# Kernel tuning notes

Measured on AMD Instinct MI355X. Metric: run time of the kernel, lower is better.

## Reference

```python
import jax, jax.numpy as jnp
import numpy as np

B, N, D = 2, 4096, 1152   # batch, tokens, txt_dim == pix_dim (num_heads = 1)
RMS_EPS = 1e-8


def setup_inputs() -> dict:
    key = jax.random.key(0)
    ks = jax.random.split(key, 8)
    w = lambda k, shape: jax.random.normal(k, shape, dtype=jnp.float32) * 0.02
    return {
        "x": jax.random.normal(ks[0], (B, N, D), dtype=jnp.float32),
        "c": jax.random.normal(ks[1], (B, N, D), dtype=jnp.float32),
        "Wqkv_pix": w(ks[2], (3 * D, D)),      # nn.Linear(pix_dim, 3*pix_dim), no bias
        "Wqkv_text": w(ks[3], (3 * D, D)),     # nn.Linear(txt_dim, 3*txt_dim), no bias
        "sq_text": jnp.ones((D,), jnp.float32),
        "sk_text": jnp.ones((D,), jnp.float32),
        "sq_pix": jnp.ones((D,), jnp.float32),
        "sk_pix": jnp.ones((D,), jnp.float32),
        "Wproj_pix": w(ks[4], (D, 2 * D)),     # nn.Linear(dim, txt_dim)
        "bproj_pix": jnp.zeros((D,), jnp.float32),
        "Wproj_text": w(ks[5], (D, 2 * D)),    # nn.Linear(dim, pix_dim)
        "bproj_text": jnp.zeros((D,), jnp.float32),
    }


def _rms_norm(t, scale):
    # RMSNorm with p<0 path: L2 norm over last dim, rms = ||x|| * d^-0.5
    d = t.shape[-1]
    rms = jnp.linalg.norm(t, axis=-1, keepdims=True) * (d ** -0.5)
    return scale * (t / (rms + RMS_EPS))


def reference(x, c, Wqkv_pix, Wqkv_text, sq_text, sk_text, sq_pix, sk_pix,
              Wproj_pix, bproj_pix, Wproj_text, bproj_text):
    Bx, Nx, D1 = x.shape  # num_heads == 1, so (B, 1, N, d) == (B, N, d)
    # pix stream QKV (from x)
    qkv_pix = (x @ Wqkv_pix.T).reshape(Bx, Nx, 3, D1)
    q_pix, k_pix, v_pix = qkv_pix[:, :, 0], qkv_pix[:, :, 1], qkv_pix[:, :, 2]
    q_pix = _rms_norm(q_pix, sq_pix)
    k_pix = _rms_norm(k_pix, sk_pix)
    # text stream QKV: NOTE the original code applies qkv_text to x, not c
    qkv_text = (x @ Wqkv_text.T).reshape(Bx, Nx, 3, D1)
    q_text, k_text, v_text = qkv_text[:, :, 0], qkv_text[:, :, 1], qkv_text[:, :, 2]
    q_text = _rms_norm(q_text, sq_text)
    k_text = _rms_norm(k_text, sk_text)
    # concat text/pix along feature dim -> (B, N, 2D)
    q = jnp.concatenate([q_text, q_pix], axis=-1)
    k = jnp.concatenate([k_text, k_pix], axis=-1)
    v = jnp.concatenate([v_text, v_pix], axis=-1)
    scale = (2 * D1) ** -0.5  # head_dim = (txt_dim + pix_dim) / num_heads
    attn = jax.nn.softmax(jnp.einsum("bnd,bmd->bnm", q, k) * scale, axis=-1)
    z = jnp.einsum("bnm,bmd->bnd", attn, v)  # (B, N, 2D)
    x_out = z @ Wproj_pix.T + bproj_pix
    c_out = z @ Wproj_text.T + bproj_text
    return (x_out, c_out)
```

## Files before the change

### kernel.cpp

```cpp
#include <hip/hip_runtime.h>
#include <hip/hip_bf16.h>
#include <stdint.h>

using short8 = __attribute__((ext_vector_type(8))) short;
using f32x4  = __attribute__((ext_vector_type(4))) float;

#define DD 1152
#define ROW 6912

static __device__ __forceinline__ float bf2f(uint32_t h){
  union { uint32_t u; float f; } v; v.u = (h & 0xffffu) << 16; return v.f;
}
static __device__ __forceinline__ ushort f2bf(float f){
  union { float f; uint32_t u; } v; v.f = f;
  uint32_t r = (v.u + 0x7fffu + ((v.u >> 16) & 1u)) >> 16;
  return (ushort)r;
}
static __device__ __forceinline__ uint32_t pack2(float a, float b){
  return (uint32_t)f2bf(a) | ((uint32_t)f2bf(b) << 16);
}

static __device__ __forceinline__ void gload16(const void* g, void* l){
  __builtin_amdgcn_global_load_lds(
      (const __attribute__((address_space(1))) void*)g,
      (__attribute__((address_space(3))) void*)l, 16, 0, 0);
}

template<int EPI>
__global__ __launch_bounds__(512, 2)
void gemm256(const ushort* __restrict__ A, int lda,
             const ushort* __restrict__ Bm, int ldb,
             void* __restrict__ Cout, int ldc,
             int K, float alpha, int ntx, int row0,
             float* __restrict__ out0, float* __restrict__ out1,
             const float* __restrict__ bias0, const float* __restrict__ bias1)
{
  __shared__ __align__(16) ushort lds[65536];
  const int tid  = threadIdx.x;
  const int w    = tid >> 6, lane = tid & 63;
  const int wr   = w >> 2, wc = w & 3;

  const int nwg = gridDim.x;
  const int wg  = blockIdx.x;
  const int swz = (wg & 7) * (nwg >> 3) + (wg >> 3);
  const int tx = swz % ntx, ty = swz / ntx;
  const int m0 = ty * 256, n0 = tx * 256;

  const int srow = lane >> 2;
  const int scol = 8 * ((lane & 3) ^ ((lane >> 3) & 3));
  const int sgA  = w * 2;
  const ushort* gA0 = A  + (size_t)(m0 + sgA * 16 + srow) * lda + scol;
  const ushort* gA1 = gA0 + (size_t)16 * lda;
  const ushort* gB0 = Bm + (size_t)(n0 + sgA * 16 + srow) * ldb + scol;
  const ushort* gB1 = gB0 + (size_t)16 * ldb;

  auto stageAll = [&](int t, int bf) {
    ushort* Lb = lds + bf * 16384;
    gload16(gA0 + t * 32, Lb + sgA * 512);
    gload16(gA1 + t * 32, Lb + sgA * 512 + 512);
    gload16(gB0 + t * 32, Lb + 8192 + sgA * 512);
    gload16(gB1 + t * 32, Lb + 8192 + sgA * 512 + 512);
  };

  const int kq    = lane >> 4;
  const int rowA0 = wr * 128 + (lane & 15);
  const int adA   = rowA0 * 32 + 8 * (kq ^ ((rowA0 >> 1) & 3));
  const int rowB0 = wc * 64 + (lane & 15);
  const int adB   = rowB0 * 32 + 8 * (kq ^ ((rowB0 >> 1) & 3));

  f32x4 acc[8][4];
#pragma unroll
  for (int m = 0; m < 8; m++)
#pragma unroll
    for (int n = 0; n < 4; n++) acc[m][n] = f32x4{0.f, 0.f, 0.f, 0.f};

  const int nt = K >> 5;

  stageAll(0, 0); stageAll(1, 1); stageAll(2, 2);
  asm volatile("s_waitcnt vmcnt(8)" ::: "memory");
  __builtin_amdgcn_s_barrier();

  for (int t = 0; t < nt; ++t) {
    const ushort* Lb = lds + (t & 3) * 16384;
    short8 a0[4], b[4];
#pragma unroll
    for (int m = 0; m < 4; m++) a0[m] = *(const short8*)(Lb + adA + m * 512);
#pragma unroll
    for (int n = 0; n < 4; n++) b[n] = *(const short8*)(Lb + 8192 + adB + n * 512);
    if (t + 3 < nt) {
      ushort* Ld = lds + ((t + 3) & 3) * 16384;
      gload16(gA0 + (t + 3) * 32, Ld + sgA * 512);
      gload16(gA1 + (t + 3) * 32, Ld + sgA * 512 + 512);
    }
    __builtin_amdgcn_s_barrier();
    __builtin_amdgcn_s_setprio(1);
#pragma unroll
    for (int m = 0; m < 4; m++)
#pragma unroll
      for (int n = 0; n < 4; n++)
        acc[m][n] = __builtin_amdgcn_mfma_f32_16x16x32_bf16(a0[m], b[n], acc[m][n], 0, 0, 0);
    __builtin_amdgcn_s_setprio(0);

    short8 a1[4];
#pragma unroll
    for (int m = 0; m < 4; m++) a1[m] = *(const short8*)(Lb + adA + (m + 4) * 512);
    if (t + 3 < nt) {
      ushort* Ld = lds + ((t + 3) & 3) * 16384;
      gload16(gB0 + (t + 3) * 32, Ld + 8192 + sgA * 512);
      gload16(gB1 + (t + 3) * 32, Ld + 8192 + sgA * 512 + 512);
    }
    if      (t + 3 < nt) asm volatile("s_waitcnt vmcnt(8)" ::: "memory");
    else if (t + 2 < nt) asm volatile("s_waitcnt vmcnt(4)" ::: "memory");
    else                 asm volatile("s_waitcnt vmcnt(0)" ::: "memory");
    __builtin_amdgcn_s_barrier();
    __builtin_amdgcn_s_setprio(1);
#pragma unroll
    for (int m = 0; m < 4; m++)
#pragma unroll
      for (int n = 0; n < 4; n++)
        acc[m + 4][n] = __builtin_amdgcn_mfma_f32_16x16x32_bf16(a1[m], b[n], acc[m + 4][n], 0, 0, 0);
    __builtin_amdgcn_s_setprio(0);
  }

#pragma unroll
  for (int m = 0; m < 8; m++) {
#pragma unroll
    for (int v = 0; v < 4; v++) {
      const int row = m0 + wr * 128 + m * 16 + (lane >> 4) * 4 + v;
#pragma unroll
      for (int n = 0; n < 4; n++) {
        const int col = n0 + wc * 64 + n * 16 + (lane & 15);
        float val = acc[m][n][v] * alpha;
        if (EPI == 0) {
          ((ushort*)Cout)[(size_t)row * ldc + col] = f2bf(val);
        } else {
          const int orow = row0 + row;
          if (col < DD) out0[(size_t)orow * DD + col] = val + bias0[col];
          else          out1[(size_t)orow * DD + (col - DD)] = val + bias1[col - DD];
        }
      }
    }
  }
}

__global__ __launch_bounds__(256)
void cvt_f32_bf16(const float* __restrict__ src, ushort* __restrict__ dst, int n4)
{
  int stride = gridDim.x * blockDim.x;
  for (int i = blockIdx.x * blockDim.x + threadIdx.x; i < n4; i += stride) {
    float4 v = ((const float4*)src)[i];
    uint2 o;
    o.x = pack2(v.x, v.y);
    o.y = pack2(v.z, v.w);
    ((uint2*)dst)[i] = o;
  }
}

__global__ __launch_bounds__(256)
void rms_inplace(ushort* __restrict__ qkv,
                 const float* __restrict__ sq_text, const float* __restrict__ sq_pix,
                 const float* __restrict__ sk_text, const float* __restrict__ sk_pix)
{
  const int row = blockIdx.x;
  const int tid = threadIdx.x, wave = tid >> 6, lane = tid & 63;
  ushort* seg = qkv + (size_t)row * ROW + wave * 1152;
  const float* scale = (wave == 0) ? sq_text : (wave == 1) ? sq_pix
                     : (wave == 2) ? sk_text : sk_pix;
  float ss = 0.f;
  for (int g = lane; g < 144; g += 64) {
    uint4 p = *(const uint4*)(seg + g * 8);
    float f0 = bf2f(p.x), f1 = bf2f(p.x >> 16), f2 = bf2f(p.y), f3 = bf2f(p.y >> 16);
    float f4 = bf2f(p.z), f5 = bf2f(p.z >> 16), f6 = bf2f(p.w), f7 = bf2f(p.w >> 16);
    ss += f0*f0 + f1*f1 + f2*f2 + f3*f3 + f4*f4 + f5*f5 + f6*f6 + f7*f7;
  }
#pragma unroll
  for (int off = 32; off; off >>= 1) ss += __shfl_xor(ss, off);
  float rms = sqrtf(ss) * 0.0294627825f;
  float inv = 1.0f / (rms + 1e-8f);
  for (int g = lane; g < 144; g += 64) {
    int d0 = g * 8;
    uint4 p = *(const uint4*)(seg + d0);
    float f[8];
    f[0]=bf2f(p.x); f[1]=bf2f(p.x>>16); f[2]=bf2f(p.y); f[3]=bf2f(p.y>>16);
    f[4]=bf2f(p.z); f[5]=bf2f(p.z>>16); f[6]=bf2f(p.w); f[7]=bf2f(p.w>>16);
    uint4 o;
    o.x = pack2(f[0]*scale[d0+0]*inv, f[1]*scale[d0+1]*inv);
    o.y = pack2(f[2]*scale[d0+2]*inv, f[3]*scale[d0+3]*inv);
    o.z = pack2(f[4]*scale[d0+4]*inv, f[5]*scale[d0+5]*inv);
    o.w = pack2(f[6]*scale[d0+6]*inv, f[7]*scale[d0+7]*inv);
    *(uint4*)(seg + d0) = o;
  }
}

__global__ __launch_bounds__(256)
void transpose_v(const ushort* __restrict__ qkv, ushort* __restrict__ Vt)
{
  __shared__ ushort t[64][72];
  const int nb = blockIdx.x, db = blockIdx.y, b = blockIdx.z;
  const int tid = threadIdx.x;
  const int d0 = db * 64;
  const int srccol = 4608 + d0;
  const int rr = tid >> 3, cc = (tid & 7) * 8;
#pragma unroll
  for (int it = 0; it < 2; it++) {
    int r = rr + it * 32;
    uint4 p = *(const uint4*)(qkv + (size_t)(b * 4096 + nb * 64 + r) * ROW + srccol + cc);
    *(uint4*)&t[r][cc] = p;
  }
  __syncthreads();
#pragma unroll
  for (int it = 0; it < 2; it++) {
    int d = rr + it * 32;
    uint4 o;
    o.x = (uint32_t)t[cc+0][d] | ((uint32_t)t[cc+1][d] << 16);
    o.y = (uint32_t)t[cc+2][d] | ((uint32_t)t[cc+3][d] << 16);
    o.z = (uint32_t)t[cc+4][d] | ((uint32_t)t[cc+5][d] << 16);
    o.w = (uint32_t)t[cc+6][d] | ((uint32_t)t[cc+7][d] << 16);
    *(uint4*)(Vt + ((size_t)b * 2304 + d0 + d) * 4096 + nb * 64 + cc) = o;
  }
}

__global__ __launch_bounds__(256)
void softmax_bf16(ushort* __restrict__ S)
{
  const int row = blockIdx.x;
  ushort* sr = S + (size_t)row * 4096;
  const int tid = threadIdx.x, wave = tid >> 6, lane = tid & 63;
  __shared__ float red[8];
  uint4 p0 = ((const uint4*)sr)[tid * 2];
  uint4 p1 = ((const uint4*)sr)[tid * 2 + 1];
  float f[16];
  f[0]=bf2f(p0.x); f[1]=bf2f(p0.x>>16); f[2]=bf2f(p0.y); f[3]=bf2f(p0.y>>16);
  f[4]=bf2f(p0.z); f[5]=bf2f(p0.z>>16); f[6]=bf2f(p0.w); f[7]=bf2f(p0.w>>16);
  f[8]=bf2f(p1.x); f[9]=bf2f(p1.x>>16); f[10]=bf2f(p1.y); f[11]=bf2f(p1.y>>16);
  f[12]=bf2f(p1.z); f[13]=bf2f(p1.z>>16); f[14]=bf2f(p1.w); f[15]=bf2f(p1.w>>16);
  float mx = f[0];
#pragma unroll
  for (int j = 1; j < 16; j++) mx = fmaxf(mx, f[j]);
#pragma unroll
  for (int off = 32; off; off >>= 1) mx = fmaxf(mx, __shfl_xor(mx, off));
  if (lane == 0) red[wave] = mx;
  __syncthreads();
  mx = fmaxf(fmaxf(red[0], red[1]), fmaxf(red[2], red[3]));
  float s = 0.f;
#pragma unroll
  for (int j = 0; j < 16; j++) { f[j] = expf(f[j] - mx); s += f[j]; }
#pragma unroll
  for (int off = 32; off; off >>= 1) s += __shfl_xor(s, off);
  if (lane == 0) red[4 + wave] = s;
  __syncthreads();
  s = red[4] + red[5] + red[6] + red[7];
  float inv = 1.0f / s;
  uint4 o0, o1;
  o0.x = pack2(f[0]*inv, f[1]*inv);  o0.y = pack2(f[2]*inv, f[3]*inv);
  o0.z = pack2(f[4]*inv, f[5]*inv);  o0.w = pack2(f[6]*inv, f[7]*inv);
  o1.x = pack2(f[8]*inv, f[9]*inv);  o1.y = pack2(f[10]*inv, f[11]*inv);
  o1.z = pack2(f[12]*inv, f[13]*inv); o1.w = pack2(f[14]*inv, f[15]*inv);
  ((uint4*)sr)[tid * 2]     = o0;
  ((uint4*)sr)[tid * 2 + 1] = o1;
}

extern "C" void kernel_launch(void* const* d_in, const int* in_sizes, int n_in,
                              void* d_out, int out_size, void* d_ws, size_t ws_size,
                              hipStream_t stream)
{
  const float* x          = (const float*)d_in[0];
  const float* Wqkv_pix   = (const float*)d_in[2];
  const float* Wqkv_text  = (const float*)d_in[3];
  const float* sq_text    = (const float*)d_in[4];
  const float* sk_text    = (const float*)d_in[5];
  const float* sq_pix     = (const float*)d_in[6];
  const float* sk_pix     = (const float*)d_in[7];
  const float* Wproj_pix  = (const float*)d_in[8];
  const float* bproj_pix  = (const float*)d_in[9];
  const float* Wproj_text = (const float*)d_in[10];
  const float* bproj_text = (const float*)d_in[11];

  if (ws_size < 195166208ULL) return;
  char* ws = (char*)d_ws;
  ushort* QKV = (ushort*)(ws);
  ushort* Z   = (ushort*)(ws);
  ushort* Vt  = (ushort*)(ws + 113246208);
  ushort* S   = (ushort*)(ws + 150994944);
  ushort* Wpb = (ushort*)(ws + 184549376);
  ushort* xb  = (ushort*)(ws + 113246208);
  ushort* Wb  = (ushort*)(ws + 150994944);

  cvt_f32_bf16<<<2048, 256, 0, stream>>>(x, xb, 9437184 / 4);
  for (int t = 0; t < 3; t++) {
    cvt_f32_bf16<<<512, 256, 0, stream>>>(Wqkv_text + (size_t)t * 1327104,
                                          Wb + (size_t)(2 * t) * 1327104, 1327104 / 4);
    cvt_f32_bf16<<<512, 256, 0, stream>>>(Wqkv_pix + (size_t)t * 1327104,
                                          Wb + (size_t)(2 * t + 1) * 1327104, 1327104 / 4);
  }
  cvt_f32_bf16<<<512, 256, 0, stream>>>(Wproj_pix, Wpb, 2654208 / 4);
  cvt_f32_bf16<<<512, 256, 0, stream>>>(Wproj_text, Wpb + 2654208, 2654208 / 4);

  gemm256<0><<<dim3(864), 512, 0, stream>>>(xb, 1152, Wb, 1152, QKV, ROW,
                                            1152, 1.0f, 27, 0,
                                            nullptr, nullptr, nullptr, nullptr);
  rms_inplace<<<8192, 256, 0, stream>>>(QKV, sq_text, sq_pix, sk_text, sk_pix);
  {
    dim3 g(64, 36, 2);
    transpose_v<<<g, 256, 0, stream>>>(QKV, Vt);
  }

  const float scale = 1.0f / 48.0f;
  const size_t slab = (size_t)4096 * ROW;
  for (int b = 0; b < 2; b++) {
    const ushort* Qb = QKV + b * slab;
    const ushort* Kb = QKV + b * slab + 2304;
    const ushort* Vb = Vt + (size_t)b * 2304 * 4096;
    ushort* Zb = Z + (size_t)b * 4096 * 2304;
    gemm256<0><<<dim3(256), 512, 0, stream>>>(Qb, ROW, Kb, ROW, S, 4096,
                                              2304, scale, 16, 0,
                                              nullptr, nullptr, nullptr, nullptr);
    softmax_bf16<<<4096, 256, 0, stream>>>(S);
    gemm256<0><<<dim3(144), 512, 0, stream>>>(S, 4096, Vb, 4096, Zb, 2304,
                                              4096, 1.0f, 9, 0,
                                              nullptr, nullptr, nullptr, nullptr);
  }

  {
    float* out0 = (float*)d_out;
    float* out1 = out0 + 9437184;
    gemm256<2><<<dim3(288), 512, 0, stream>>>(Z, 2304, Wpb, 2304, nullptr, 0,
                                              2304, 1.0f, 9, 0,
                                              out0, out1, bproj_pix, bproj_text);
  }
}
```

Baseline: 755.3 us.

## Restructure GEMM main loop into four-quadrant schedule with K=64 tiles

Rewrites the 256x256 GEMM inner loop to use K-steps of 64 with the tile split into four 128x128 quadrants. Each quadrant is computed by all waves in turn while the next half-tiles stream into double-buffered LDS with a new XOR swizzle. This interleaves global loads with MFMA phases more finely and halves the number of loop iterations. It adds more barriers per iteration and changes the wave-to-output mapping, which could hurt if synchronisation dominates.

```diff
diff --git a/kernel.cpp b/kernel.cpp
--- a/kernel.cpp
+++ b/kernel.cpp
@@ -46,97 +46,151 @@
   const int tx = swz % ntx, ty = swz / ntx;
   const int m0 = ty * 256, n0 = tx * 256;
 
-  const int srow = lane >> 2;
-  const int scol = 8 * ((lane & 3) ^ ((lane >> 3) & 3));
-  const int sgA  = w * 2;
-  const ushort* gA0 = A  + (size_t)(m0 + sgA * 16 + srow) * lda + scol;
-  const ushort* gA1 = gA0 + (size_t)16 * lda;
-  const ushort* gB0 = Bm + (size_t)(n0 + sgA * 16 + srow) * ldb + scol;
-  const ushort* gB1 = gB0 + (size_t)16 * ldb;
-
-  auto stageAll = [&](int t, int bf) {
-    ushort* Lb = lds + bf * 16384;
-    gload16(gA0 + t * 32, Lb + sgA * 512);
-    gload16(gA1 + t * 32, Lb + sgA * 512 + 512);
-    gload16(gB0 + t * 32, Lb + 8192 + sgA * 512);
-    gload16(gB1 + t * 32, Lb + 8192 + sgA * 512 + 512);
+  const int sr = lane >> 3;
+  const int cc = 8 * ((lane & 7) ^ sr);
+  auto stageA = [&](int h, int tt) {
+    ushort* Ld = lds + ((tt & 1) * 2 + h) * 8192 + w * 1024;
+    const ushort* g = A + (size_t)(m0 + h * 128 + w * 16 + sr) * lda + tt * 64 + cc;
+    gload16(g, Ld);
+    gload16(g + (size_t)8 * lda, Ld + 512);
   };
-
-  const int kq    = lane >> 4;
-  const int rowA0 = wr * 128 + (lane & 15);
-  const int adA   = rowA0 * 32 + 8 * (kq ^ ((rowA0 >> 1) & 3));
-  const int rowB0 = wc * 64 + (lane & 15);
-  const int adB   = rowB0 * 32 + 8 * (kq ^ ((rowB0 >> 1) & 3));
-
-  f32x4 acc[8][4];
-#pragma unroll
-  for (int m = 0; m < 8; m++)
-#pragma unroll
-    for (int n = 0; n < 4; n++) acc[m][n] = f32x4{0.f, 0.f, 0.f, 0.f};
-
-  const int nt = K >> 5;
-
-  stageAll(0, 0); stageAll(1, 1); stageAll(2, 2);
-  asm volatile("s_waitcnt vmcnt(8)" ::: "memory");
+  auto stageB = [&](int h, int tt) {
+    ushort* Ld = lds + 32768 + ((tt & 1) * 2 + h) * 8192 + w * 1024;
+    const ushort* g = Bm + (size_t)(n0 + h * 128 + w * 16 + sr) * ldb + tt * 64 + cc;
+    gload16(g, Ld);
+    gload16(g + (size_t)8 * ldb, Ld + 512);
+  };
+
+  const int rowA = (wr * 64 + (lane & 15)) * 64;
+  const int rowB = (wc * 32 + (lane & 15)) * 64;
+  const int ck0  = 8 * (((lane >> 4) + 0) ^ (lane & 7));
+  const int ck1  = 8 * (((lane >> 4) + 4) ^ (lane & 7));
+
+  f32x4 acc0[4][2], acc1[4][2], acc2[4][2], acc3[4][2];
+#pragma unroll
+  for (int m = 0; m < 4; m++)
+#pragma unroll
+    for (int n = 0; n < 2; n++) {
+      acc0[m][n] = f32x4{0.f,0.f,0.f,0.f}; acc1[m][n] = f32x4{0.f,0.f,0.f,0.f};
+      acc2[m][n] = f32x4{0.f,0.f,0.f,0.f}; acc3[m][n] = f32x4{0.f,0.f,0.f,0.f};
+    }
+
+  const int nt = K >> 6;
+
+  stageA(0, 0); stageB(0, 0); stageA(1, 0); stageB(1, 0);
+  stageA(0, 1); stageB(0, 1);
+  asm volatile("s_waitcnt vmcnt(4)" ::: "memory");
   __builtin_amdgcn_s_barrier();
 
   for (int t = 0; t < nt; ++t) {
-    const ushort* Lb = lds + (t & 3) * 16384;
-    short8 a0[4], b[4];
-#pragma unroll
-    for (int m = 0; m < 4; m++) a0[m] = *(const short8*)(Lb + adA + m * 512);
-#pragma unroll
-    for (int n = 0; n < 4; n++) b[n] = *(const short8*)(Lb + 8192 + adB + n * 512);
-    if (t + 3 < nt) {
-      ushort* Ld = lds + ((t + 3) & 3) * 16384;
-      gload16(gA0 + (t + 3) * 32, Ld + sgA * 512);
-      gload16(gA1 + (t + 3) * 32, Ld + sgA * 512 + 512);
-    }
+    const ushort* LA = lds + (t & 1) * 16384;
+    const ushort* LB = LA + 32768;
+    short8 a[4][2], b[2][2];
+
+#pragma unroll
+    for (int m = 0; m < 4; m++) {
+      a[m][0] = *(const short8*)(LA + rowA + m * 1024 + ck0);
+      a[m][1] = *(const short8*)(LA + rowA + m * 1024 + ck1);
+    }
+#pragma unroll
+    for (int n = 0; n < 2; n++) {
+      b[n][0] = *(const short8*)(LB + rowB + n * 1024 + ck0);
+      b[n][1] = *(const short8*)(LB + rowB + n * 1024 + ck1);
+    }
+    if (t + 1 < nt) stageA(1, t + 1);
     __builtin_amdgcn_s_barrier();
     __builtin_amdgcn_s_setprio(1);
 #pragma unroll
     for (int m = 0; m < 4; m++)
 #pragma unroll
-      for (int n = 0; n < 4; n++)
-        acc[m][n] = __builtin_amdgcn_mfma_f32_16x16x32_bf16(a0[m], b[n], acc[m][n], 0, 0, 0);
+      for (int n = 0; n < 2; n++) {
+        acc0[m][n] = __builtin_amdgcn_mfma_f32_16x16x32_bf16(a[m][0], b[n][0], acc0[m][n], 0, 0, 0);
+        acc0[m][n] = __builtin_amdgcn_mfma_f32_16x16x32_bf16(a[m][1], b[n][1], acc0[m][n], 0, 0, 0);
+      }
     __builtin_amdgcn_s_setprio(0);
-
-    short8 a1[4];
-#pragma unroll
-    for (int m = 0; m < 4; m++) a1[m] = *(const short8*)(Lb + adA + (m + 4) * 512);
-    if (t + 3 < nt) {
-      ushort* Ld = lds + ((t + 3) & 3) * 16384;
-      gload16(gB0 + (t + 3) * 32, Ld + 8192 + sgA * 512);
-      gload16(gB1 + (t + 3) * 32, Ld + 8192 + sgA * 512 + 512);
-    }
-    if      (t + 3 < nt) asm volatile("s_waitcnt vmcnt(8)" ::: "memory");
-    else if (t + 2 < nt) asm volatile("s_waitcnt vmcnt(4)" ::: "memory");
-    else                 asm volatile("s_waitcnt vmcnt(0)" ::: "memory");
+    __builtin_amdgcn_s_barrier();
+
+#pragma unroll
+    for (int m = 0; m < 4; m++) {
+      a[m][0] = *(const short8*)(LA + 8192 + rowA + m * 1024 + ck0);
+      a[m][1] = *(const short8*)(LA + 8192 + rowA + m * 1024 + ck1);
+    }
+    if (t + 1 < nt) stageB(1, t + 1);
     __builtin_amdgcn_s_barrier();
     __builtin_amdgcn_s_setprio(1);
 #pragma unroll
     for (int m = 0; m < 4; m++)
 #pragma unroll
-      for (int n = 0; n < 4; n++)
-        acc[m + 4][n] = __builtin_amdgcn_mfma_f32_16x16x32_bf16(a1[m], b[n], acc[m + 4][n], 0, 0, 0);
+      for (int n = 0; n < 2; n++) {
+        acc1[m][n] = __builtin_amdgcn_mfma_f32_16x16x32_bf16(a[m][0], b[n][0], acc1[m][n], 0, 0, 0);
+        acc1[m][n] = __builtin_amdgcn_mfma_f32_16x16x32_bf16(a[m][1], b[n][1], acc1[m][n], 0, 0, 0);
+      }
     __builtin_amdgcn_s_setprio(0);
-  }
-
-#pragma unroll
-  for (int m = 0; m < 8; m++) {
-#pragma unroll
-    for (int v = 0; v < 4; v++) {
-      const int row = m0 + wr * 128 + m * 16 + (lane >> 4) * 4 + v;
-#pragma unroll
-      for (int n = 0; n < 4; n++) {
-        const int col = n0 + wc * 64 + n * 16 + (lane & 15);
-        float val = acc[m][n][v] * alpha;
-        if (EPI == 0) {
-          ((ushort*)Cout)[(size_t)row * ldc + col] = f2bf(val);
-        } else {
-          const int orow = row0 + row;
-          if (col < DD) out0[(size_t)orow * DD + col] = val + bias0[col];
-          else          out1[(size_t)orow * DD + (col - DD)] = val + bias1[col - DD];
+    __builtin_amdgcn_s_barrier();
+
+#pragma unroll
+    for (int m = 0; m < 4; m++) {
+      a[m][0] = *(const short8*)(LA + rowA + m * 1024 + ck0);
+      a[m][1] = *(const short8*)(LA + rowA + m * 1024 + ck1);
+    }
+#pragma unroll
+    for (int n = 0; n < 2; n++) {
+      b[n][0] = *(const short8*)(LB + 8192 + rowB + n * 1024 + ck0);
+      b[n][1] = *(const short8*)(LB + 8192 + rowB + n * 1024 + ck1);
+    }
+    if (t + 2 < nt) stageB(0, t + 2);
+    __builtin_amdgcn_s_barrier();
+    __builtin_amdgcn_s_setprio(1);
+#pragma unroll
+    for (int m = 0; m < 4; m++)
+#pragma unroll
+      for (int n = 0; n < 2; n++) {
+        acc2[m][n] = __builtin_amdgcn_mfma_f32_16x16x32_bf16(a[m][0], b[n][0], acc2[m][n], 0, 0, 0);
+        acc2[m][n] = __builtin_amdgcn_mfma_f32_16x16x32_bf16(a[m][1], b[n][1], acc2[m][n], 0, 0, 0);
+      }
+    __builtin_amdgcn_s_setprio(0);
+    __builtin_amdgcn_s_barrier();
+
+#pragma unroll
+    for (int m = 0; m < 4; m++) {
+      a[m][0] = *(const short8*)(LA + 8192 + rowA + m * 1024 + ck0);
+      a[m][1] = *(const short8*)(LA + 8192 + rowA + m * 1024 + ck1);
+    }
+    if (t + 2 < nt) stageA(0, t + 2);
+    asm volatile("s_waitcnt vmcnt(4)" ::: "memory");
+    __builtin_amdgcn_s_barrier();
+    __builtin_amdgcn_s_setprio(1);
+#pragma unroll
+    for (int m = 0; m < 4; m++)
+#pragma unroll
+      for (int n = 0; n < 2; n++) {
+        acc3[m][n] = __builtin_amdgcn_mfma_f32_16x16x32_bf16(a[m][0], b[n][0], acc3[m][n], 0, 0, 0);
+        acc3[m][n] = __builtin_amdgcn_mfma_f32_16x16x32_bf16(a[m][1], b[n][1], acc3[m][n], 0, 0, 0);
+      }
+    __builtin_amdgcn_s_setprio(0);
+    __builtin_amdgcn_s_barrier();
+  }
+
+#pragma unroll
+  for (int q = 0; q < 4; q++) {
+    const int MH = q & 1, NH = q >> 1;
+    f32x4 (*ac)[2] = (q == 0) ? acc0 : (q == 1) ? acc1 : (q == 2) ? acc2 : acc3;
+#pragma unroll
+    for (int m = 0; m < 4; m++) {
+#pragma unroll
+      for (int v = 0; v < 4; v++) {
+        const int row = m0 + MH * 128 + wr * 64 + m * 16 + (lane >> 4) * 4 + v;
+#pragma unroll
+        for (int n = 0; n < 2; n++) {
+          const int col = n0 + NH * 128 + wc * 32 + n * 16 + (lane & 15);
+          float val = ac[m][n][v] * alpha;
+          if (EPI == 0) {
+            ((ushort*)Cout)[(size_t)row * ldc + col] = f2bf(val);
+          } else {
+            const int orow = row0 + row;
+            if (col < DD) out0[(size_t)orow * DD + col] = val + bias0[col];
+            else          out1[(size_t)orow * DD + (col - DD)] = val + bias1[col - DD];
+          }
         }
       }
     }
```

Measured after the change: 813.4 us. 1.08x slower.
